# Kernel optimization log

Measured on AMD Instinct MI355X. Metric: run time of the kernel, lower is better.

The kernel has to match this reference:

```python
import jax, jax.numpy as jnp
import numpy as np

S = 64.0   # margin_loss scale
M2 = 0.5   # arcface additive angular margin (m1=1.0, m3=0.0)
EPS = 1e-7

BATCH = 1024
EMB = 512
NUM_CLASSES = 200000


def setup_inputs() -> dict:
    key = jax.random.key(0)
    k1, k2, k3 = jax.random.split(key, 3)
    embeddings = jax.random.normal(k1, (BATCH, EMB), dtype=jnp.float32)
    weight = jax.random.normal(k2, (NUM_CLASSES, EMB), dtype=jnp.float32) * 0.01
    labels = jax.random.randint(k3, (BATCH,), 0, NUM_CLASSES, dtype=jnp.int64)
    return {"embeddings": embeddings, "weight": weight, "labels": labels}


def reference(embeddings, weight, labels):
    # L2 normalize rows (torch.nn.functional.normalize, eps=1e-12)
    ne = embeddings / jnp.maximum(jnp.linalg.norm(embeddings, axis=1, keepdims=True), 1e-12)
    nw = weight / jnp.maximum(jnp.linalg.norm(weight, axis=1, keepdims=True), 1e-12)
    # cosine logits [B, C], clamped to [-1, 1]
    logits = jnp.clip(jnp.einsum('be,ce->bc', ne, nw), -1.0, 1.0)
    B = logits.shape[0]
    rows = jnp.arange(B)
    lbl = labels.astype(jnp.int32)
    # arcface margin: cos(theta + m2) applied only at the target class
    target = logits[rows, lbl]
    final_target = jnp.cos(jnp.arccos(jnp.clip(target, -1.0 + EPS, 1.0 - EPS)) + M2)
    logits = logits.at[rows, lbl].set(final_target) * S
    # mean cross-entropy
    logp = jax.nn.log_softmax(logits, axis=1)
    return -jnp.mean(logp[rows, lbl])
```

## Files before the change

kernel.cpp:

```cpp
#include <hip/hip_runtime.h>
#include <math.h>


#define S_SCALE 64.0f
#define MARGIN2 0.5f
#define EPSS 1e-7f

#define BATCH 1024
#define EMB 512
#define NCLS 200000

#define BM 256
#define BN 128
#define BK 32
#define NCHUNKS ((NCLS + BN - 1) / BN)
#define NCLS_PAD (NCHUNKS * BN)

typedef __bf16 bf16x8 __attribute__((ext_vector_type(8)));
typedef float floatx4 __attribute__((ext_vector_type(4)));

#define OFF_NEBF 0
#define LEN_NEBF (BATCH * EMB / 2)
#define OFF_WINV (OFF_NEBF + LEN_NEBF)
#define LEN_WINV 200192
#define OFF_PL (OFF_WINV + LEN_WINV)
#define LEN_P (BATCH * NCHUNKS)
#define OFF_TSV (OFF_PL + LEN_P)
#define OFF_RL (OFF_TSV + BATCH)
#define OFF_WBF (OFF_RL + BATCH)
#define LEN_WBF ((size_t)NCLS_PAD * EMB / 2)
#define NEED_BYTES (((size_t)OFF_WBF + LEN_WBF) * 4)

__device__ inline ushort f2bf(float f) {
    unsigned u = __float_as_uint(f);
    unsigned r = (u + 0x7FFFu + ((u >> 16) & 1u)) >> 16;
    return (ushort)r;
}

__device__ __forceinline__ void gload_lds16(const void* g, void* l) {
    __builtin_amdgcn_global_load_lds(
        (const __attribute__((address_space(1))) void*)g,
        (__attribute__((address_space(3))) void*)l, 16, 0, 0);
}

__global__ void norm_emb_kernel(const float* __restrict__ e, ushort* __restrict__ nebf) {
    int r = blockIdx.x;
    int t = threadIdx.x;
    float v0 = e[r * EMB + t];
    float v1 = e[r * EMB + t + 256];
    __shared__ float red[256];
    red[t] = v0 * v0 + v1 * v1;
    __syncthreads();
    for (int o = 128; o > 0; o >>= 1) {
        if (t < o) red[t] += red[t + o];
        __syncthreads();
    }
    float inv = 1.0f / fmaxf(sqrtf(red[0]), 1e-12f);
    nebf[r * EMB + t] = f2bf(v0 * inv);
    nebf[r * EMB + t + 256] = f2bf(v1 * inv);
}

__global__ void norm_w_kernel(const float* __restrict__ w, ushort* __restrict__ wbf) {
    int tid = threadIdx.x;
    int wv = tid >> 6, lane = tid & 63;
    int row = blockIdx.x * 4 + wv;
    const float* wr = w + (size_t)row * EMB;
    float4 v0 = *(const float4*)(wr + lane * 4);
    float4 v1 = *(const float4*)(wr + lane * 4 + 256);
    float ss = v0.x * v0.x + v0.y * v0.y + v0.z * v0.z + v0.w * v0.w
             + v1.x * v1.x + v1.y * v1.y + v1.z * v1.z + v1.w * v1.w;
#pragma unroll
    for (int m = 32; m >= 1; m >>= 1) ss += __shfl_xor(ss, m);
    float inv = 1.0f / fmaxf(sqrtf(ss), 1e-12f);
    ushort* dst = wbf + (size_t)row * EMB;
    ushort4 p0, p1;
    p0.x = f2bf(v0.x * inv); p0.y = f2bf(v0.y * inv);
    p0.z = f2bf(v0.z * inv); p0.w = f2bf(v0.w * inv);
    p1.x = f2bf(v1.x * inv); p1.y = f2bf(v1.y * inv);
    p1.z = f2bf(v1.z * inv); p1.w = f2bf(v1.w * inv);
    *(ushort4*)(dst + lane * 4) = p0;
    *(ushort4*)(dst + lane * 4 + 256) = p1;
}

__global__ void winv_kernel(const float* __restrict__ w, float* __restrict__ winv) {
    int tid = threadIdx.x;
    int wv = tid >> 6, lane = tid & 63;
    int row = blockIdx.x * 4 + wv;
    const float* wr = w + (size_t)row * EMB;
    float ss = 0.f;
#pragma unroll
    for (int q = 0; q < 8; ++q) {
        float v = wr[lane + 64 * q];
        ss += v * v;
    }
#pragma unroll
    for (int m = 32; m >= 1; m >>= 1) ss += __shfl_xor(ss, m);
    if (lane == 0) winv[row] = 1.0f / fmaxf(sqrtf(ss), 1e-12f);
}

template <bool PRE>
__global__ __launch_bounds__(512) void gemm_lse_kernel(
    const ushort* __restrict__ nebf, const ushort* __restrict__ wbf,
    const float* __restrict__ w, const float* __restrict__ winv,
    const int* __restrict__ labels,
    float* __restrict__ pl, float* __restrict__ tsv) {
    __shared__ ushort Als[BM * 32];
    __shared__ ushort Bls[BN * 32];
    __shared__ float psum[2][BM];

    const int tid = threadIdx.x;
    const int rowBase = blockIdx.x * BM;
    const int colBase = blockIdx.y * BN;
    const int lane = tid & 63, wv = tid >> 6;
    const int wave_m = wv & 3, wave_n = wv >> 2;
    const int lr = lane & 15, quad = lane >> 4;

    const int srow = lane >> 2, skoff = (lane & 3) * 8;
    const int bcol = tid >> 2, bq = tid & 3;
    const int bcls = colBase + bcol;
    const bool bvalid = bcls < NCLS;

    floatx4 acc[4][4];
#pragma unroll
    for (int i = 0; i < 4; i++)
#pragma unroll
        for (int j = 0; j < 4; j++) acc[i][j] = (floatx4){0.f, 0.f, 0.f, 0.f};

    const ushort* aseg0 = nebf + (size_t)(rowBase + wv * 32 + srow) * EMB + skoff;
    const ushort* aseg1 = aseg0 + (size_t)16 * EMB;
    const ushort* bseg = PRE ? (wbf + (size_t)(colBase + wv * 16 + srow) * EMB + skoff) : (const ushort*)0;
    ushort* albase0 = &Als[(wv * 32) * 32];
    ushort* albase1 = &Als[(wv * 32 + 16) * 32];
    ushort* blbase = &Bls[(wv * 16) * 32];

    for (int kt = 0; kt < EMB; kt += BK) {
        gload_lds16(aseg0 + kt, albase0);
        gload_lds16(aseg1 + kt, albase1);
        if (PRE) {
            gload_lds16(bseg + kt, blbase);
        } else {
            float4 v0 = make_float4(0.f, 0.f, 0.f, 0.f);
            float4 v1 = make_float4(0.f, 0.f, 0.f, 0.f);
            if (bvalid) {
                const float* src = w + (size_t)bcls * EMB + kt + bq * 8;
                v0 = *(const float4*)(src);
                v1 = *(const float4*)(src + 4);
            }
            union { ushort us[8]; uint4 v; } pk;
            pk.us[0] = f2bf(v0.x); pk.us[1] = f2bf(v0.y);
            pk.us[2] = f2bf(v0.z); pk.us[3] = f2bf(v0.w);
            pk.us[4] = f2bf(v1.x); pk.us[5] = f2bf(v1.y);
            pk.us[6] = f2bf(v1.z); pk.us[7] = f2bf(v1.w);
            *(uint4*)&Bls[bcol * 32 + bq * 8] = pk.v;
        }
        __syncthreads();

        bf16x8 af[4], bfr[4];
#pragma unroll
        for (int i = 0; i < 4; i++)
            af[i] = *(const bf16x8*)&Als[(wave_m * 64 + i * 16 + lr) * 32 + quad * 8];
#pragma unroll
        for (int j = 0; j < 4; j++)
            bfr[j] = *(const bf16x8*)&Bls[(wave_n * 64 + j * 16 + lr) * 32 + quad * 8];
#pragma unroll
        for (int i = 0; i < 4; i++)
#pragma unroll
            for (int j = 0; j < 4; j++)
                acc[i][j] = __builtin_amdgcn_mfma_f32_16x16x32_bf16(af[i], bfr[j], acc[i][j], 0, 0, 0);
        __syncthreads();
    }

    float wvv[4];
    if (!PRE) {
#pragma unroll
        for (int j = 0; j < 4; j++) {
            int gc = colBase + wave_n * 64 + j * 16 + lr;
            wvv[j] = (gc < NCLS) ? winv[gc] : 0.f;
        }
    }
#pragma unroll
    for (int i = 0; i < 4; i++) {
#pragma unroll
        for (int r = 0; r < 4; r++) {
            int rowloc = wave_m * 64 + i * 16 + quad * 4 + r;
            int grow = rowBase + rowloc;
            int lbl = labels[grow];
            float s = 0.f;
#pragma unroll
            for (int j = 0; j < 4; j++) {
                int gc = colBase + wave_n * 64 + j * 16 + lr;
                if (gc < NCLS) {
                    float c = PRE ? acc[i][j][r] : acc[i][j][r] * wvv[j];
                    c = fminf(fmaxf(c, -1.f), 1.f);
                    if (gc == lbl) {
                        float tt = fminf(fmaxf(c, -1.f + EPSS), 1.f - EPSS);
                        c = __cosf(acosf(tt) + MARGIN2);
                        tsv[grow] = c * S_SCALE;
                    }
                    s += __expf(c * S_SCALE - S_SCALE);
                }
            }
#pragma unroll
            for (int m = 1; m < 16; m <<= 1) s += __shfl_xor(s, m);
            if (lr == 0) psum[wave_n][rowloc] = s;
        }
    }
    __syncthreads();
    if (tid < BM) {
        size_t grow = rowBase + tid;
        pl[grow * NCHUNKS + blockIdx.y] = psum[0][tid] + psum[1][tid];
    }
}

__global__ void chunk_reduce_kernel(const float* __restrict__ pl,
                                    const float* __restrict__ tsv, float* __restrict__ rowloss) {
    int r = blockIdx.x, t = threadIdx.x;
    const float* l = pl + (size_t)r * NCHUNKS;
    __shared__ float red[256];
    float s = 0.f;
    for (int i = t; i < NCHUNKS; i += 256) s += l[i];
    red[t] = s;
    __syncthreads();
    for (int o = 128; o > 0; o >>= 1) {
        if (t < o) red[t] += red[t + o];
        __syncthreads();
    }
    if (t == 0) rowloss[r] = S_SCALE + logf(red[0]) - tsv[r];
}

__global__ void final_kernel(const float* __restrict__ rowloss, float* __restrict__ out) {
    int t = threadIdx.x;
    float s = 0.f;
    for (int i = t; i < BATCH; i += 256) s += rowloss[i];
    __shared__ float red[256];
    red[t] = s;
    __syncthreads();
    for (int o = 128; o > 0; o >>= 1) {
        if (t < o) red[t] += red[t + o];
        __syncthreads();
    }
    if (t == 0) out[0] = red[0] / (float)BATCH;
}

extern "C" void kernel_launch(void* const* d_in, const int* in_sizes, int n_in,
                              void* d_out, int out_size, void* d_ws, size_t ws_size,
                              hipStream_t stream) {
    const float* emb = (const float*)d_in[0];
    const float* w = (const float*)d_in[1];
    const int* labels = (const int*)d_in[2];
    float* ws = (float*)d_ws;
    ushort* nebf = (ushort*)(ws + OFF_NEBF);
    float* winv = ws + OFF_WINV;
    float* pl = ws + OFF_PL;
    float* tsv = ws + OFF_TSV;
    float* rl = ws + OFF_RL;
    ushort* wbf = (ushort*)(ws + OFF_WBF);

    const bool pre = ws_size >= NEED_BYTES;

    norm_emb_kernel<<<BATCH, 256, 0, stream>>>(emb, nebf);
    dim3 grid(BATCH / BM, NCHUNKS);
    if (pre) {
        norm_w_kernel<<<NCLS / 4, 256, 0, stream>>>(w, wbf);
        gemm_lse_kernel<true><<<grid, 512, 0, stream>>>(nebf, wbf, w, winv, labels, pl, tsv);
    } else {
        winv_kernel<<<NCLS / 4, 256, 0, stream>>>(w, winv);
        gemm_lse_kernel<false><<<grid, 512, 0, stream>>>(nebf, wbf, w, winv, labels, pl, tsv);
    }
    chunk_reduce_kernel<<<BATCH, 256, 0, stream>>>(pl, tsv, rl);
    final_kernel<<<1, 256, 0, stream>>>(rl, (float*)d_out);
}
```

Measured before the change: 895.6 us.

## Double-buffer LDS tiles, swizzle LDS layout, and remap blocks across XCDs

Splits the A and B shared-memory tiles into two buffers so the next K-slice is loaded while MFMAs run on the current one, leaving one barrier per iteration instead of two. Applies an XOR swizzle to the LDS column offsets to cut bank conflicts on fragment reads. Remaps block indices so that blocks placed on the same XCD work on neighbouring class chunks, which should improve L2 reuse of weight rows. Doubling the LDS footprint may lower occupancy.

```diff
diff --git a/kernel.cpp b/kernel.cpp
--- a/kernel.cpp
+++ b/kernel.cpp
@@ -15,6 +15,7 @@
 #define BK 32
 #define NCHUNKS ((NCLS + BN - 1) / BN)
 #define NCLS_PAD (NCHUNKS * BN)
+#define NBLK (4 * NCHUNKS)
 
 typedef __bf16 bf16x8 __attribute__((ext_vector_type(8)));
 typedef float floatx4 __attribute__((ext_vector_type(4)));
@@ -104,19 +105,31 @@
     const float* __restrict__ w, const float* __restrict__ winv,
     const int* __restrict__ labels,
     float* __restrict__ pl, float* __restrict__ tsv) {
-    __shared__ ushort Als[BM * 32];
-    __shared__ ushort Bls[BN * 32];
+    __shared__ ushort Als[2][BM * 32];
+    __shared__ ushort Bls[2][BN * 32];
     __shared__ float psum[2][BM];
 
     const int tid = threadIdx.x;
-    const int rowBase = blockIdx.x * BM;
-    const int colBase = blockIdx.y * BN;
+
+    const int d = blockIdx.y * 4 + blockIdx.x;
+    const int xcd = d & 7, slot = d >> 3;
+    const int qq = NBLK >> 3, rr = NBLK & 7;
+    const int logical =
+        ((xcd < rr) ? xcd * (qq + 1) : rr * (qq + 1) + (xcd - rr) * qq) + slot;
+    const int rowBase = (logical & 3) * BM;
+    const int chunk = logical >> 2;
+    const int colBase = chunk * BN;
+
     const int lane = tid & 63, wv = tid >> 6;
     const int wave_m = wv & 3, wave_n = wv >> 2;
     const int lr = lane & 15, quad = lane >> 4;
 
-    const int srow = lane >> 2, skoff = (lane & 3) * 8;
+    const int srow = lane >> 2;
+    const int skoff = (((lane & 3) ^ ((srow >> 1) & 3)) * 8);
+    const int rq = (quad ^ ((lr >> 1) & 3)) * 8;
+
     const int bcol = tid >> 2, bq = tid & 3;
+    const int bslot = ((bq ^ ((bcol >> 1) & 3)) * 8);
     const int bcls = colBase + bcol;
     const bool bvalid = bcls < NCLS;
 
@@ -129,20 +142,47 @@
     const ushort* aseg0 = nebf + (size_t)(rowBase + wv * 32 + srow) * EMB + skoff;
     const ushort* aseg1 = aseg0 + (size_t)16 * EMB;
     const ushort* bseg = PRE ? (wbf + (size_t)(colBase + wv * 16 + srow) * EMB + skoff) : (const ushort*)0;
-    ushort* albase0 = &Als[(wv * 32) * 32];
-    ushort* albase1 = &Als[(wv * 32 + 16) * 32];
-    ushort* blbase = &Bls[(wv * 16) * 32];
-
-    for (int kt = 0; kt < EMB; kt += BK) {
-        gload_lds16(aseg0 + kt, albase0);
-        gload_lds16(aseg1 + kt, albase1);
-        if (PRE) {
-            gload_lds16(bseg + kt, blbase);
-        } else {
+
+#define STAGE_A(b, kt)                                                 \
+    do {                                                               \
+        gload_lds16(aseg0 + (kt), &Als[b][(wv * 32) * 32]);            \
+        gload_lds16(aseg1 + (kt), &Als[b][(wv * 32 + 16) * 32]);       \
+    } while (0)
+#define STAGE_B(b, kt) gload_lds16(bseg + (kt), &Bls[b][(wv * 16) * 32])
+#define COMPUTE(b)                                                                    \
+    do {                                                                              \
+        bf16x8 af[4], bfr[4];                                                         \
+        _Pragma("unroll") for (int i = 0; i < 4; i++)                                 \
+            af[i] = *(const bf16x8*)&Als[b][(wave_m * 64 + i * 16 + lr) * 32 + rq];   \
+        _Pragma("unroll") for (int j = 0; j < 4; j++)                                 \
+            bfr[j] = *(const bf16x8*)&Bls[b][(wave_n * 64 + j * 16 + lr) * 32 + rq];  \
+        _Pragma("unroll") for (int i = 0; i < 4; i++)                                 \
+            _Pragma("unroll") for (int j = 0; j < 4; j++)                             \
+                acc[i][j] = __builtin_amdgcn_mfma_f32_16x16x32_bf16(af[i], bfr[j],    \
+                                                                    acc[i][j], 0, 0, 0); \
+    } while (0)
+
+    if (PRE) {
+        STAGE_A(0, 0);
+        STAGE_B(0, 0);
+        __syncthreads();
+        int cur = 0;
+#pragma unroll
+        for (int kt = BK; kt < EMB; kt += BK) {
+            STAGE_A(cur ^ 1, kt);
+            STAGE_B(cur ^ 1, kt);
+            COMPUTE(cur);
+            __syncthreads();
+            cur ^= 1;
+        }
+        COMPUTE(cur);
+    } else {
+        {
+            STAGE_A(0, 0);
             float4 v0 = make_float4(0.f, 0.f, 0.f, 0.f);
             float4 v1 = make_float4(0.f, 0.f, 0.f, 0.f);
             if (bvalid) {
-                const float* src = w + (size_t)bcls * EMB + kt + bq * 8;
+                const float* src = w + (size_t)bcls * EMB + bq * 8;
                 v0 = *(const float4*)(src);
                 v1 = *(const float4*)(src + 4);
             }
@@ -151,24 +191,35 @@
             pk.us[2] = f2bf(v0.z); pk.us[3] = f2bf(v0.w);
             pk.us[4] = f2bf(v1.x); pk.us[5] = f2bf(v1.y);
             pk.us[6] = f2bf(v1.z); pk.us[7] = f2bf(v1.w);
-            *(uint4*)&Bls[bcol * 32 + bq * 8] = pk.v;
-        }
-        __syncthreads();
-
-        bf16x8 af[4], bfr[4];
-#pragma unroll
-        for (int i = 0; i < 4; i++)
-            af[i] = *(const bf16x8*)&Als[(wave_m * 64 + i * 16 + lr) * 32 + quad * 8];
-#pragma unroll
-        for (int j = 0; j < 4; j++)
-            bfr[j] = *(const bf16x8*)&Bls[(wave_n * 64 + j * 16 + lr) * 32 + quad * 8];
-#pragma unroll
-        for (int i = 0; i < 4; i++)
-#pragma unroll
-            for (int j = 0; j < 4; j++)
-                acc[i][j] = __builtin_amdgcn_mfma_f32_16x16x32_bf16(af[i], bfr[j], acc[i][j], 0, 0, 0);
-        __syncthreads();
-    }
+            *(uint4*)&Bls[0][bcol * 32 + bslot] = pk.v;
+            __syncthreads();
+        }
+        int cur = 0;
+#pragma unroll
+        for (int kt = BK; kt < EMB; kt += BK) {
+            STAGE_A(cur ^ 1, kt);
+            float4 v0 = make_float4(0.f, 0.f, 0.f, 0.f);
+            float4 v1 = make_float4(0.f, 0.f, 0.f, 0.f);
+            if (bvalid) {
+                const float* src = w + (size_t)bcls * EMB + kt + bq * 8;
+                v0 = *(const float4*)(src);
+                v1 = *(const float4*)(src + 4);
+            }
+            COMPUTE(cur);
+            union { ushort us[8]; uint4 v; } pk;
+            pk.us[0] = f2bf(v0.x); pk.us[1] = f2bf(v0.y);
+            pk.us[2] = f2bf(v0.z); pk.us[3] = f2bf(v0.w);
+            pk.us[4] = f2bf(v1.x); pk.us[5] = f2bf(v1.y);
+            pk.us[6] = f2bf(v1.z); pk.us[7] = f2bf(v1.w);
+            *(uint4*)&Bls[cur ^ 1][bcol * 32 + bslot] = pk.v;
+            __syncthreads();
+            cur ^= 1;
+        }
+        COMPUTE(cur);
+    }
+#undef STAGE_A
+#undef STAGE_B
+#undef COMPUTE
 
     float wvv[4];
     if (!PRE) {
@@ -208,7 +259,7 @@
     __syncthreads();
     if (tid < BM) {
         size_t grow = rowBase + tid;
-        pl[grow * NCHUNKS + blockIdx.y] = psum[0][tid] + psum[1][tid];
+        pl[grow * NCHUNKS + chunk] = psum[0][tid] + psum[1][tid];
     }
 }
 
```

Measured after the change: 861.5 us. -3.8%, faster.
